# Optimization experiments

Measured on AMD Instinct MI355X. Metric: run time of the kernel, lower is better.

The kernel has to match this reference:

```python
import jax, jax.numpy as jnp
import numpy as np

B, N, D, OUT = 4, 512, 128, 128

def setup_inputs() -> dict:
    key = jax.random.key(0)
    k1, k2, k3, k4 = jax.random.split(key, 4)
    x = jax.random.normal(k1, (B, N, D), dtype=jnp.float32)
    # binary adjacency mask (float, as it multiplies edge features in the original)
    adj = (jax.random.uniform(k2, (B, N, N)) < 0.5).astype(jnp.float32)
    # nn.Linear(2D, OUT): store as (2D, OUT) so y = feat @ W + b
    W = jax.random.normal(k3, (2 * D, OUT), dtype=jnp.float32) * (1.0 / np.sqrt(2 * D))
    b = jax.random.normal(k4, (OUT,), dtype=jnp.float32) * 0.01
    return {"x": x, "adj": adj, "W": W, "b": b}

def reference(x, adj, W, b):
    # edge_feat = cat([x_i, x_j - x_i]); linear on concat decomposes as
    # x_i @ W1 + (x_j - x_i) @ W2 = x_i @ (W1 - W2) + x_j @ W2  -> avoids the (B,N,N,2D) concat.
    d = x.shape[-1]
    W1, W2 = W[:d], W[d:]
    p = jnp.einsum('bnd,do->bno', x, W1 - W2)   # contribution of x_i
    q = jnp.einsum('bnd,do->bno', x, W2)        # contribution of x_j
    pre = p[:, :, None, :] + q[:, None, :, :] + b  # (B, N, N, OUT)
    h = jax.nn.relu(pre) * adj[..., None]          # dropout is identity in eval mode
    return jnp.max(h, axis=2)                      # max over neighbors j -> (B, N, OUT)
```

## Files before the change

kernel.cpp:

```cpp
#include <hip/hip_runtime.h>

#define B_ 4
#define N_ 512
#define D_ 128
#define O_ 128

#define R1 8

__global__ __launch_bounds__(512)
void gemm_pq_kernel(const float* __restrict__ x, const float* __restrict__ W,
                    const float* __restrict__ bias, float* __restrict__ q,
                    float* __restrict__ phat) {
    const int tid = threadIdx.x;
    const int o   = tid & (O_ - 1);
    const int kq  = __builtin_amdgcn_readfirstlane(tid >> 7);
    const int row0 = blockIdx.x * R1;

    const float* __restrict__ xb = x + (size_t)row0 * D_;

    float accp[R1], accq[R1];
#pragma unroll
    for (int r = 0; r < R1; ++r) { accp[r] = 0.0f; accq[r] = 0.0f; }

    const int k0 = kq * (D_ / 4);
#pragma unroll 4
    for (int k = k0; k < k0 + D_ / 4; ++k) {
        const float w1 = W[(size_t)k * O_ + o];
        const float w2 = W[(size_t)(k + D_) * O_ + o];
        const float wd = w1 - w2;
#pragma unroll
        for (int r = 0; r < R1; ++r) {
            const float xv = xb[(size_t)r * D_ + k];
            accp[r] = fmaf(xv, wd, accp[r]);
            accq[r] = fmaf(xv, w2, accq[r]);
        }
    }

    __shared__ float red[R1][O_][5];

#pragma unroll
    for (int r = 0; r < R1; ++r) red[r][o][kq] = accq[r];
    __syncthreads();
    {
        for (int t = tid; t < R1 * O_; t += 512) {
            const int r = t >> 7, oo = t & (O_ - 1);
            const float s = (red[r][oo][0] + red[r][oo][1]) +
                            (red[r][oo][2] + red[r][oo][3]);
            q[(size_t)(row0 + r) * O_ + oo] = s;
        }
    }
    __syncthreads();
#pragma unroll
    for (int r = 0; r < R1; ++r) red[r][o][kq] = accp[r];
    __syncthreads();
    {
        for (int t = tid; t < R1 * O_; t += 512) {
            const int r = t >> 7, oo = t & (O_ - 1);
            const float s = (red[r][oo][0] + red[r][oo][1]) +
                            (red[r][oo][2] + red[r][oo][3]);
            phat[(size_t)(row0 + r) * O_ + oo] = s + bias[oo];
        }
    }
}

#define TI 8
#define JS 8

__global__ __launch_bounds__(1024)
void maskmax_kernel(const float* __restrict__ q, const float* __restrict__ phat,
                    const float* __restrict__ adj, float* __restrict__ out) {
    const int tid = threadIdx.x;
    const int o   = tid & (O_ - 1);
    const int jq  = __builtin_amdgcn_readfirstlane(tid >> 7);
    const int b   = blockIdx.x >> 6;
    const int i0  = (blockIdx.x & 63) * TI;

    const float* __restrict__ qb   = q + (size_t)b * N_ * O_ + o;
    const float* __restrict__ arow = adj + ((size_t)b * N_ + i0) * N_;

    float m[TI];
#pragma unroll
    for (int i = 0; i < TI; ++i) m[i] = -1e30f;

    const int j0 = jq * (N_ / JS);
    for (int j = j0; j < j0 + (N_ / JS); j += 8) {
        float qv[8];
#pragma unroll
        for (int u = 0; u < 8; ++u)
            qv[u] = qb[(size_t)(j + u) * O_];
#pragma unroll
        for (int i = 0; i < TI; ++i) {
            const float* __restrict__ ar = arow + (size_t)i * N_ + j;
            const float c0 = fmaf(ar[0], 1024.0f, qv[0]);
            const float c1 = fmaf(ar[1], 1024.0f, qv[1]);
            const float c2 = fmaf(ar[2], 1024.0f, qv[2]);
            const float c3 = fmaf(ar[3], 1024.0f, qv[3]);
            const float c4 = fmaf(ar[4], 1024.0f, qv[4]);
            const float c5 = fmaf(ar[5], 1024.0f, qv[5]);
            const float c6 = fmaf(ar[6], 1024.0f, qv[6]);
            const float c7 = fmaf(ar[7], 1024.0f, qv[7]);
            float mi = m[i];
            mi = fmaxf(mi, fmaxf(c0, c1));
            mi = fmaxf(mi, fmaxf(c2, c3));
            mi = fmaxf(mi, fmaxf(c4, c5));
            mi = fmaxf(mi, fmaxf(c6, c7));
            m[i] = mi;
        }
    }

    __shared__ float part[TI][O_][JS + 1];
#pragma unroll
    for (int i = 0; i < TI; ++i) part[i][o][jq] = m[i];
    __syncthreads();

    {
        const int i  = tid >> 7;
        const int oo = tid & (O_ - 1);
        float mm = -1e30f;
#pragma unroll
        for (int p = 0; p < JS; ++p) mm = fmaxf(mm, part[i][oo][p]);
        const size_t idx = ((size_t)b * N_ + i0 + i) * O_ + oo;
        const float v = phat[idx] + mm - 1024.0f;
        out[idx] = v > 0.0f ? v : 0.0f;
    }
}

extern "C" void kernel_launch(void* const* d_in, const int* in_sizes, int n_in,
                              void* d_out, int out_size, void* d_ws, size_t ws_size,
                              hipStream_t stream) {
    const float* x    = (const float*)d_in[0];
    const float* adj  = (const float*)d_in[1];
    const float* W    = (const float*)d_in[2];
    const float* bias = (const float*)d_in[3];
    float* out = (float*)d_out;

    float* q    = (float*)d_ws;
    float* phat = q + (size_t)B_ * N_ * O_;

    gemm_pq_kernel<<<(B_ * N_) / R1, 512, 0, stream>>>(x, W, bias, q, phat);
    maskmax_kernel<<<B_ * (N_ / TI), 1024, 0, stream>>>(q, phat, adj, out);
}
```

Measured before the change: 75.51 us.

## Fuse GEMM and masked-max into one cooperative kernel with grid sync

Merges the projection GEMM and the masked neighbor-max kernels into a single cooperative launch of 256 blocks of 1024 threads, with a grid-wide sync between the two phases. Each block keeps its own phat rows in registers instead of writing and re-reading them from global memory. Only q is shared through the workspace. This removes one kernel launch and the phat round trip, but adds grid-sync and threadfence overhead. It also depends on all 256 blocks being co-resident, and the GEMM phase now splits K across 8 groups.

```diff
diff --git a/kernel.cpp b/kernel.cpp
--- a/kernel.cpp
+++ b/kernel.cpp
@@ -1,79 +1,77 @@
 #include <hip/hip_runtime.h>
+#include <hip/hip_cooperative_groups.h>
+
+namespace cg = cooperative_groups;
 
 #define B_ 4
 #define N_ 512
 #define D_ 128
 #define O_ 128
+#define TI 8
+#define JS 8
 
-#define R1 8
-
-__global__ __launch_bounds__(512)
-void gemm_pq_kernel(const float* __restrict__ x, const float* __restrict__ W,
-                    const float* __restrict__ bias, float* __restrict__ q,
-                    float* __restrict__ phat) {
+__global__ __launch_bounds__(1024)
+void fused_edgeconv_kernel(const float* __restrict__ x,
+                           const float* __restrict__ adj,
+                           const float* __restrict__ W,
+                           const float* __restrict__ bias,
+                           float* __restrict__ q,
+                           float* __restrict__ out) {
     const int tid = threadIdx.x;
     const int o   = tid & (O_ - 1);
-    const int kq  = __builtin_amdgcn_readfirstlane(tid >> 7);
-    const int row0 = blockIdx.x * R1;
+    const int g8  = __builtin_amdgcn_readfirstlane(tid >> 7);
+    const int b   = blockIdx.x >> 6;
+    const int i0  = (blockIdx.x & 63) * TI;
+    const int row0 = b * N_ + i0;
+
+    __shared__ float red[TI][O_][JS + 1];
 
     const float* __restrict__ xb = x + (size_t)row0 * D_;
 
-    float accp[R1], accq[R1];
+    float accp[TI], accq[TI];
 #pragma unroll
-    for (int r = 0; r < R1; ++r) { accp[r] = 0.0f; accq[r] = 0.0f; }
+    for (int r = 0; r < TI; ++r) { accp[r] = 0.0f; accq[r] = 0.0f; }
 
-    const int k0 = kq * (D_ / 4);
+    const int k0 = g8 * (D_ / JS);
 #pragma unroll 4
-    for (int k = k0; k < k0 + D_ / 4; ++k) {
+    for (int k = k0; k < k0 + D_ / JS; ++k) {
         const float w1 = W[(size_t)k * O_ + o];
         const float w2 = W[(size_t)(k + D_) * O_ + o];
         const float wd = w1 - w2;
 #pragma unroll
-        for (int r = 0; r < R1; ++r) {
+        for (int r = 0; r < TI; ++r) {
             const float xv = xb[(size_t)r * D_ + k];
             accp[r] = fmaf(xv, wd, accp[r]);
             accq[r] = fmaf(xv, w2, accq[r]);
         }
     }
 
-    __shared__ float red[R1][O_][5];
+    const int rr = tid >> 7;
+    const int oo = tid & (O_ - 1);
 
 #pragma unroll
-    for (int r = 0; r < R1; ++r) red[r][o][kq] = accq[r];
+    for (int r = 0; r < TI; ++r) red[r][o][g8] = accq[r];
     __syncthreads();
     {
-        for (int t = tid; t < R1 * O_; t += 512) {
-            const int r = t >> 7, oo = t & (O_ - 1);
-            const float s = (red[r][oo][0] + red[r][oo][1]) +
-                            (red[r][oo][2] + red[r][oo][3]);
-            q[(size_t)(row0 + r) * O_ + oo] = s;
-        }
+        const float s = ((red[rr][oo][0] + red[rr][oo][1]) +
+                         (red[rr][oo][2] + red[rr][oo][3])) +
+                        ((red[rr][oo][4] + red[rr][oo][5]) +
+                         (red[rr][oo][6] + red[rr][oo][7]));
+        q[(size_t)(row0 + rr) * O_ + oo] = s;
     }
     __syncthreads();
+
 #pragma unroll
-    for (int r = 0; r < R1; ++r) red[r][o][kq] = accp[r];
+    for (int r = 0; r < TI; ++r) red[r][o][g8] = accp[r];
     __syncthreads();
-    {
-        for (int t = tid; t < R1 * O_; t += 512) {
-            const int r = t >> 7, oo = t & (O_ - 1);
-            const float s = (red[r][oo][0] + red[r][oo][1]) +
-                            (red[r][oo][2] + red[r][oo][3]);
-            phat[(size_t)(row0 + r) * O_ + oo] = s + bias[oo];
-        }
-    }
-}
+    const float phat_reg = ((red[rr][oo][0] + red[rr][oo][1]) +
+                            (red[rr][oo][2] + red[rr][oo][3])) +
+                           ((red[rr][oo][4] + red[rr][oo][5]) +
+                            (red[rr][oo][6] + red[rr][oo][7])) + bias[oo];
 
-#define TI 8
-#define JS 8
-
-__global__ __launch_bounds__(1024)
-void maskmax_kernel(const float* __restrict__ q, const float* __restrict__ phat,
-                    const float* __restrict__ adj, float* __restrict__ out) {
-    const int tid = threadIdx.x;
-    const int o   = tid & (O_ - 1);
-    const int jq  = __builtin_amdgcn_readfirstlane(tid >> 7);
-    const int b   = blockIdx.x >> 6;
-    const int i0  = (blockIdx.x & 63) * TI;
+    __threadfence();
+    cg::this_grid().sync();
+    __threadfence();
 
     const float* __restrict__ qb   = q + (size_t)b * N_ * O_ + o;
     const float* __restrict__ arow = adj + ((size_t)b * N_ + i0) * N_;
@@ -82,7 +80,7 @@
 #pragma unroll
     for (int i = 0; i < TI; ++i) m[i] = -1e30f;
 
-    const int j0 = jq * (N_ / JS);
+    const int j0 = g8 * (N_ / JS);
     for (int j = j0; j < j0 + (N_ / JS); j += 8) {
         float qv[8];
 #pragma unroll
@@ -108,20 +106,16 @@
         }
     }
 
-    __shared__ float part[TI][O_][JS + 1];
 #pragma unroll
-    for (int i = 0; i < TI; ++i) part[i][o][jq] = m[i];
+    for (int i = 0; i < TI; ++i) red[i][o][g8] = m[i];
     __syncthreads();
 
     {
-        const int i  = tid >> 7;
-        const int oo = tid & (O_ - 1);
         float mm = -1e30f;
 #pragma unroll
-        for (int p = 0; p < JS; ++p) mm = fmaxf(mm, part[i][oo][p]);
-        const size_t idx = ((size_t)b * N_ + i0 + i) * O_ + oo;
-        const float v = phat[idx] + mm - 1024.0f;
-        out[idx] = v > 0.0f ? v : 0.0f;
+        for (int p = 0; p < JS; ++p) mm = fmaxf(mm, red[rr][oo][p]);
+        const float v = phat_reg + mm - 1024.0f;
+        out[(size_t)(row0 + rr) * O_ + oo] = v > 0.0f ? v : 0.0f;
     }
 }
 
@@ -134,9 +128,11 @@
     const float* bias = (const float*)d_in[3];
     float* out = (float*)d_out;
 
-    float* q    = (float*)d_ws;
-    float* phat = q + (size_t)B_ * N_ * O_;
+    float* q = (float*)d_ws;
 
-    gemm_pq_kernel<<<(B_ * N_) / R1, 512, 0, stream>>>(x, W, bias, q, phat);
-    maskmax_kernel<<<B_ * (N_ / TI), 1024, 0, stream>>>(q, phat, adj, out);
+    void* args[] = { (void*)&x, (void*)&adj, (void*)&W, (void*)&bias,
+                     (void*)&q, (void*)&out };
+    hipLaunchCooperativeKernel((const void*)fused_edgeconv_kernel,
+                               dim3(B_ * (N_ / TI)), dim3(1024),
+                               args, 0, stream);
 }
```

Measured after the change: 231.5 us. +206.6%, slower.
